# Kernel optimization log

Measured on AMD Instinct MI355X. Metric: run time of the kernel, lower is better.

The kernel has to match this reference:

```python
import jax, jax.numpy as jnp
import numpy as np

B, C, H, W = 64, 1024, 14, 14
DK, DV, NH = 512, 512, 8
NCLS = 32  # each class appears B//NCLS = 2 times -> no singleton labels


def setup_inputs() -> dict:
    key = jax.random.key(0)
    k1, k2, k3, k4 = jax.random.split(key, 4)
    dkh = DK // NH
    x = jax.random.normal(k1, (B, C, H, W), jnp.float32)
    W_qkv = jax.random.normal(k2, (2 * DK + DV, C), jnp.float32) * 0.02
    b_qkv = jnp.zeros((2 * DK + DV,), jnp.float32)
    key_rel_w = jax.random.normal(k3, (2 * W - 1, dkh), jnp.float32)
    key_rel_h = jax.random.normal(k4, (2 * H - 1, dkh), jnp.float32)
    # label-based pair index (training path of the torch module)
    rng = np.random.default_rng(0)
    labels = np.repeat(np.arange(NCLS), B // NCLS)
    rng.shuffle(labels)
    pair = np.empty(B, np.int32)
    for j in range(B):
        idx = np.nonzero(labels == labels[j])[0]
        pos = int(np.nonzero(idx == j)[0][0])
        pair[j] = idx[(pos + 1) % len(idx)]
    return {"x": x, "W_qkv": W_qkv, "b_qkv": b_qkv,
            "key_rel_w": key_rel_w, "key_rel_h": key_rel_h,
            "pair_index": jnp.asarray(pair)}


def rel_to_abs(x):
    b, nh, L, _ = x.shape
    x = jnp.pad(x, ((0, 0), (0, 0), (0, 0), (0, 1)))            # [b,nh,L,2L]
    flat = x.reshape(b, nh, L * 2 * L)
    flat = jnp.pad(flat, ((0, 0), (0, 0), (0, L - 1)))
    return flat.reshape(b, nh, L + 1, 2 * L - 1)[:, :, :L, L - 1:]


def relative_logits_1d(q, rel_k, Hd, Wd, nh, case):
    # q: [b, nh, Hd, Wd, dkh]; rel_k: [2*Wd-1, dkh]
    b = q.shape[0]
    rel = jnp.einsum('bhxyd,md->bhxym', q, rel_k)                 # [b,nh,Hd,Wd,2Wd-1]
    rel = rel_to_abs(rel.reshape(b, nh * Hd, Wd, 2 * Wd - 1))     # [b,nh*Hd,Wd,Wd]
    rel = rel.reshape(b, nh, Hd, Wd, Wd)[:, :, :, None]           # [b,nh,Hd,1,Wd,Wd]
    rel = jnp.broadcast_to(rel, (b, nh, Hd, Hd, Wd, Wd))
    if case == 'w':
        rel = jnp.swapaxes(rel, 3, 4)
    else:  # 'h'
        rel = jnp.swapaxes(rel, 2, 4)
        rel = jnp.swapaxes(rel, 4, 5)
        rel = jnp.swapaxes(rel, 3, 5)
    return rel.reshape(b, nh, Hd * Wd, Hd * Wd)


def reference(x, W_qkv, b_qkv, key_rel_w, key_rel_h, pair_index):
    b, c, h, w = x.shape
    nh, dk, dv = NH, DK, DV
    dkh = dk // nh
    # 1x1 conv == channel GEMM
    qkv = jnp.einsum('bchw,oc->bohw', x, W_qkv) + b_qkv[None, :, None, None]
    q = qkv[:, :dk].reshape(b, nh, dkh, h, w) * dkh ** (-0.5)
    k = qkv[:, dk:2 * dk].reshape(b, nh, dkh, h, w)
    flat_q = q.reshape(b, nh, dkh, h * w)
    flat_k = k.reshape(b, nh, dkh, h * w)
    flat_q = flat_q / jnp.linalg.norm(flat_q, axis=2, keepdims=True)
    flat_k = flat_k / jnp.linalg.norm(flat_k, axis=2, keepdims=True)
    q_avg = (flat_q[pair_index] + flat_q) * 0.5
    logits = jnp.einsum('bndq,bndk->bnqk', q_avg, flat_k)         # [b,nh,HW,HW]
    q_perm = jnp.transpose(q, (0, 1, 3, 4, 2))                    # [b,nh,h,w,dkh]
    w_rel = relative_logits_1d(q_perm, key_rel_w, h, w, nh, 'w')
    h_rel = relative_logits_1d(jnp.swapaxes(q_perm, 2, 3), key_rel_h, w, h, nh, 'h')
    logits = logits + h_rel + w_rel
    # combine_heads + mean over dim 1 == mean over (nh, query) axes
    mean_logits = jnp.mean(logits.reshape(b, nh, h * w, h, w), axis=(1, 2))  # [b,h,w]
    attn = jax.nn.softmax(mean_logits.reshape(b, -1), axis=-1).reshape(b, 1, h, w)
    return jnp.concatenate((x / 49.0, x * attn), axis=1)
```

## Files before the change

### kernel.cpp

```cpp
#include <hip/hip_runtime.h>
#include <hip/hip_bf16.h>
#include <math.h>

typedef unsigned short ushort_t;
using bf16x8 = __attribute__((ext_vector_type(8))) short;
using f32x4  = __attribute__((ext_vector_type(4))) float;

#define BATCH 64
#define CIN   1024
#define HH    14
#define WW    14
#define P     196
#define NHEAD 8
#define DKH   64
#define PPAD  224

#define OFF_Y16  0
#define N_Y16_F  6422528
#define OFF_XB   (OFF_Y16 + N_Y16_F)
#define N_XB_F   7340032
#define OFF_WB   (OFF_XB + N_XB_F)
#define N_WB_F   524288
#define OFF_INK  (OFF_WB + N_WB_F)
#define N_INK    (BATCH*NHEAD*P)
#define OFF_SQ   (OFF_INK + N_INK)
#define N_SQ     (BATCH*NHEAD*DKH)
#define OFF_QHP  (OFF_SQ + N_SQ)
#define N_QHP    (BATCH*NHEAD*HH*DKH)
#define OFF_QWP  (OFF_QHP + N_QHP)
#define N_QWP    (BATCH*NHEAD*WW*DKH)
#define OFF_DOTP (OFF_QWP + N_QWP)
#define N_DOTP   (BATCH*NHEAD*P)
#define OFF_ATTN (OFF_DOTP + N_DOTP)
#define N_ATTN   (BATCH*P)

__device__ __forceinline__ ushort_t f2bf(float f) {
    union { float f; unsigned u; } v; v.f = f;
    unsigned r = v.u + 0x7fffu + ((v.u >> 16) & 1u);
    return (ushort_t)(r >> 16);
}
__device__ __forceinline__ float bf2f(ushort_t u) {
    union { unsigned u; float f; } v; v.u = ((unsigned)u) << 16; return v.f;
}
__device__ __forceinline__ void gll16(const ushort_t* g, ushort_t* l) {
    __builtin_amdgcn_global_load_lds(
        (const __attribute__((address_space(1))) void*)g,
        (__attribute__((address_space(3))) void*)l, 16, 0, 0);
}

__global__ __launch_bounds__(256) void k_convW(const float* __restrict__ Wq,
                                               ushort_t* __restrict__ Wb) {
    int i = blockIdx.x * 256 + threadIdx.x;
    const float4 v = ((const float4*)Wq)[i];
    ushort4 o;
    o.x = f2bf(v.x); o.y = f2bf(v.y); o.z = f2bf(v.z); o.w = f2bf(v.w);
    ((ushort4*)Wb)[i] = o;
}

__global__ __launch_bounds__(256) void k_trans(const float* __restrict__ x,
                                               ushort_t* __restrict__ Xb) {
    const int c0 = blockIdx.x * 64, p0 = blockIdx.y * 32, b = blockIdx.z;
    const int t = threadIdx.x;
    __shared__ float tile[64][33];
    const float* xb = x + (size_t)b * (CIN * P);
#pragma unroll
    for (int it = 0; it < 8; ++it) {
        int idx = t + it * 256;
        int c_l = idx >> 5, p_l = idx & 31;
        int p = p0 + p_l;
        tile[c_l][p_l] = (p < P) ? xb[(size_t)(c0 + c_l) * P + p] : 0.f;
    }
    __syncthreads();
    int c_chunk = (t & 7) * 8, p_l = t >> 3;
    ushort_t buf[8];
#pragma unroll
    for (int e = 0; e < 8; ++e) buf[e] = f2bf(tile[c_chunk + e][p_l]);
    *(uint4*)(Xb + ((size_t)b * PPAD + p0 + p_l) * CIN + c0 + c_chunk) = *(uint4*)buf;
}

__global__ __launch_bounds__(256, 4) void k_mfma(const ushort_t* __restrict__ Xb,
                                                 const ushort_t* __restrict__ Wb,
                                                 const float* __restrict__ bias,
                                                 ushort_t* __restrict__ Y16) {
    const int o0 = blockIdx.x * 128, r0 = blockIdx.y * 128;
    const int tid = threadIdx.x, w = tid >> 6, l = tid & 63;
    const int wm = w >> 1, wn = w & 1;
    __shared__ ushort_t xa[128 * 64];
    __shared__ ushort_t xw[128 * 64];
    f32x4 acc[4][4];
#pragma unroll
    for (int mf = 0; mf < 4; ++mf)
#pragma unroll
        for (int j = 0; j < 4; ++j) acc[mf][j] = (f32x4){0.f, 0.f, 0.f, 0.f};

    const ushort_t* Ab = Xb + (size_t)r0 * CIN;
    const ushort_t* Bb = Wb + (size_t)o0 * CIN;
    const int lrow = l >> 3, lch = (l & 7) * 8;

    for (int c0 = 0; c0 < CIN; c0 += 64) {
        if (c0) __syncthreads();
#pragma unroll
        for (int i = 0; i < 4; ++i) {
            int rowblk = (w * 4 + i) * 8;
            gll16(Ab + (size_t)(rowblk + lrow) * CIN + c0 + lch, xa + rowblk * 64);
        }
#pragma unroll
        for (int i = 0; i < 4; ++i) {
            int rowblk = (w * 4 + i) * 8;
            gll16(Bb + (size_t)(rowblk + lrow) * CIN + c0 + lch, xw + rowblk * 64);
        }
        __syncthreads();
#pragma unroll
        for (int kk = 0; kk < 2; ++kk) {
            bf16x8 bfrag[4];
#pragma unroll
            for (int j = 0; j < 4; ++j)
                bfrag[j] = *(const bf16x8*)(xw + (wn * 64 + j * 16 + (l & 15)) * 64 + kk * 32 + (l >> 4) * 8);
#pragma unroll
            for (int mf = 0; mf < 4; ++mf) {
                bf16x8 afrag = *(const bf16x8*)(xa + (wm * 64 + mf * 16 + (l & 15)) * 64 + kk * 32 + (l >> 4) * 8);
#pragma unroll
                for (int j = 0; j < 4; ++j)
                    acc[mf][j] = __builtin_amdgcn_mfma_f32_16x16x32_bf16(afrag, bfrag[j], acc[mf][j], 0, 0, 0);
            }
        }
    }
    const int oc = l & 15, pq = (l >> 4) * 4;
#pragma unroll
    for (int j = 0; j < 4; ++j) {
        int o = o0 + wn * 64 + j * 16 + oc;
        float bo = bias[o];
#pragma unroll
        for (int mf = 0; mf < 4; ++mf) {
            int r = r0 + wm * 64 + mf * 16 + pq;
            int b = r / PPAD;
            int p = r - b * PPAD;
            if (p < P) {
                ushort_t tmp[4];
#pragma unroll
                for (int e = 0; e < 4; ++e) tmp[e] = f2bf(acc[mf][j][e] + bo);
                *(ushort4*)(Y16 + ((size_t)b * 1024 + o) * P + p) = *(ushort4*)tmp;
            }
        }
    }
}

__global__ __launch_bounds__(256) void k_norm(const ushort_t* __restrict__ Y16,
                                              float* __restrict__ ink_g,
                                              float* __restrict__ sq_g,
                                              float* __restrict__ qhp,
                                              float* __restrict__ qwp) {
    const int bn = blockIdx.x, b = bn >> 3, n = bn & 7;
    const int tid = threadIdx.x;
    __shared__ ushort_t qs[64 * P];
    __shared__ float inq_s[P];
    __shared__ float part[4][64];
    const uint* Yq = (const uint*)(Y16 + ((size_t)b * 1024 + n * 64) * P);
    for (int i = tid; i < 64 * (P / 2); i += 256) ((uint*)qs)[i] = Yq[i];
    const ushort_t* Yk = Y16 + ((size_t)b * 1024 + 512 + n * 64) * P;
    const int p = tid, pc = (p < P) ? p : 0;
    float sk = 0.f;
    for (int d = 0; d < 64; ++d) { float v = bf2f(Yk[d * P + pc]); sk = fmaf(v, v, sk); }
    __syncthreads();
    float sq = 0.f;
    for (int d = 0; d < 64; ++d) { float v = bf2f(qs[d * P + pc]); sq = fmaf(v, v, sq); }
    if (p < P) { ink_g[bn * P + p] = rsqrtf(sk); inq_s[p] = rsqrtf(sq); }
    __syncthreads();
    {
        int d = tid & 63, q4 = tid >> 6;
        float s = 0.f;
        for (int i = 0; i < 49; ++i) {
            int pp = q4 * 49 + i;
            s = fmaf(bf2f(qs[d * P + pp]), inq_s[pp], s);
        }
        part[q4][d] = s;
    }
    __syncthreads();
    if (tid < 64) sq_g[bn * 64 + tid] = part[0][tid] + part[1][tid] + part[2][tid] + part[3][tid];
    for (int it = tid; it < 896; it += 256) {
        int d = it & 63, xx = it >> 6;
        float s = 0.f;
#pragma unroll
        for (int y = 0; y < WW; ++y) s += bf2f(qs[d * P + xx * WW + y]);
        qhp[bn * 896 + it] = s * 0.125f;
    }
    for (int it = tid; it < 896; it += 256) {
        int d = it & 63, y = it >> 6;
        float s = 0.f;
#pragma unroll
        for (int xx = 0; xx < HH; ++xx) s += bf2f(qs[d * P + xx * WW + y]);
        qwp[bn * 896 + it] = s * 0.125f;
    }
}

__global__ __launch_bounds__(256) void k_dot(const ushort_t* __restrict__ Y16,
                                             const float* __restrict__ ink_g,
                                             const float* __restrict__ sq_g,
                                             const int*   __restrict__ pair,
                                             float* __restrict__ dotp) {
    const int bn = blockIdx.x, b = bn >> 3, n = bn & 7;
    const int tid = threadIdx.x;
    __shared__ float Sav[64];
    if (tid < 64) {
        int pb = pair[b];
        Sav[tid] = 0.5f * (sq_g[bn * 64 + tid] + sq_g[(pb * 8 + n) * 64 + tid]);
    }
    __syncthreads();
    const int p = tid;
    if (p < P) {
        const ushort_t* Yk = Y16 + ((size_t)b * 1024 + 512 + n * 64) * P;
        float s = 0.f;
#pragma unroll 8
        for (int d = 0; d < 64; ++d) s = fmaf(Sav[d], bf2f(Yk[d * P + p]), s);
        dotp[bn * P + p] = s * ink_g[bn * P + p];
    }
}

__global__ __launch_bounds__(256) void k_attn2(const float* __restrict__ dotp,
                                               const float* __restrict__ qhp,
                                               const float* __restrict__ qwp,
                                               const float* __restrict__ relw,
                                               const float* __restrict__ relh,
                                               float* __restrict__ attn_g) {
    const int b = blockIdx.x, tid = threadIdx.x;
    __shared__ float qhs[896], qws[896];
    __shared__ float Aw[WW], Ah[HH];
    __shared__ float red[256];
    for (int i = tid; i < 896; i += 256) {
        float sh = 0.f, sw = 0.f;
#pragma unroll
        for (int n = 0; n < 8; ++n) {
            sh += qhp[(size_t)(b * 8 + n) * 896 + i];
            sw += qwp[(size_t)(b * 8 + n) * 896 + i];
        }
        qhs[i] = sh; qws[i] = sw;
    }
    if (tid < WW) { Aw[tid] = 0.f; Ah[tid] = 0.f; }
    __syncthreads();
    if (tid < 196) {
        int X = tid / 14, y = tid % 14;
        const float* qp = &qws[y * 64];
        const float* rw = relw + (13 + X - y) * 64;
        float s = 0.f;
#pragma unroll 8
        for (int d = 0; d < 64; ++d) s = fmaf(qp[d], rw[d], s);
        atomicAdd(&Aw[X], s);
        const float* hp = &qhs[y * 64];
        const float* rh = relh + (13 + X - y) * 64;
        float s2 = 0.f;
#pragma unroll 8
        for (int d = 0; d < 64; ++d) s2 = fmaf(hp[d], rh[d], s2);
        atomicAdd(&Ah[X], s2);
    }
    __syncthreads();
    const int p = tid;
    float v = -1e30f;
    if (p < P) {
        float dot = 0.f;
#pragma unroll
        for (int n = 0; n < 8; ++n) dot += dotp[(size_t)(b * 8 + n) * P + p];
        v = (dot + Ah[p / WW] + Aw[p % WW]) * (1.f / 1568.f);
    }
    red[tid] = v; __syncthreads();
    for (int s = 128; s > 0; s >>= 1) { if (tid < s) red[tid] = fmaxf(red[tid], red[tid + s]); __syncthreads(); }
    float mx = red[0]; __syncthreads();
    float e = (p < P) ? expf(v - mx) : 0.f;
    red[tid] = e; __syncthreads();
    for (int s = 128; s > 0; s >>= 1) { if (tid < s) red[tid] += red[tid + s]; __syncthreads(); }
    if (p < P) attn_g[b * P + p] = e / red[0];
}

__global__ __launch_bounds__(256) void k_out(const float* __restrict__ x,
                                             const float* __restrict__ attn_g,
                                             float* __restrict__ out) {
    const int total4 = BATCH * CIN * P / 4;
    const int stride = gridDim.x * 256;
    const float4* x4 = (const float4*)x;
    const float4* a4 = (const float4*)attn_g;
    float4* o4 = (float4*)out;
    for (int i4 = blockIdx.x * 256 + threadIdx.x; i4 < total4; i4 += stride) {
        int i = i4 * 4;
        int b = i / (CIN * P);
        int r = i - b * (CIN * P);
        int p0 = r % P;
        float4 xv = x4[i4];
        float4 at = a4[(b * P + p0) >> 2];
        float4 o1 = make_float4(xv.x * (1.f/49.f), xv.y * (1.f/49.f),
                                xv.z * (1.f/49.f), xv.w * (1.f/49.f));
        float4 o2 = make_float4(xv.x * at.x, xv.y * at.y, xv.z * at.z, xv.w * at.w);
        o4[(b * (2 * CIN * P) + r) >> 2] = o1;
        o4[(b * (2 * CIN * P) + CIN * P + r) >> 2] = o2;
    }
}

extern "C" void kernel_launch(void* const* d_in, const int* in_sizes, int n_in,
                              void* d_out, int out_size, void* d_ws, size_t ws_size,
                              hipStream_t stream) {
    const float* x    = (const float*)d_in[0];
    const float* Wq   = (const float*)d_in[1];
    const float* bias = (const float*)d_in[2];
    const float* relw = (const float*)d_in[3];
    const float* relh = (const float*)d_in[4];
    const int*   pair = (const int*)d_in[5];
    float* out = (float*)d_out;
    float* ws  = (float*)d_ws;

    ushort_t* Y16 = (ushort_t*)(ws + OFF_Y16);
    ushort_t* Xb  = (ushort_t*)(ws + OFF_XB);
    ushort_t* Wb  = (ushort_t*)(ws + OFF_WB);
    float* ink  = ws + OFF_INK;
    float* sq   = ws + OFF_SQ;
    float* qhp  = ws + OFF_QHP;
    float* qwp  = ws + OFF_QWP;
    float* dotp = ws + OFF_DOTP;
    float* attn = ws + OFF_ATTN;

    k_convW<<<1024, 256, 0, stream>>>(Wq, Wb);
    k_trans<<<dim3(16, 7, 64), 256, 0, stream>>>(x, Xb);
    k_mfma <<<dim3(8, 112), 256, 0, stream>>>(Xb, Wb, bias, Y16);
    k_norm <<<BATCH * NHEAD, 256, 0, stream>>>(Y16, ink, sq, qhp, qwp);
    k_dot  <<<BATCH * NHEAD, 256, 0, stream>>>(Y16, ink, sq, pair, dotp);
    k_attn2<<<BATCH, 256, 0, stream>>>(dotp, qhp, qwp, relw, relh, attn);
    k_out  <<<2048, 256, 0, stream>>>(x, attn, out);
}
```

Measured before the change: 118.6 us.

## Merge weight/input conversion kernels and fuse norm with pair dot product

Combines the weight bf16 conversion and the input transpose into one launch by splitting on block index. It also fuses the normalization and dot kernels: each block now loads its paired sample's query tile and recomputes that tile's normalized sum locally, instead of passing ink/sq through global memory. This removes two launches and a dependency, at the cost of doubling query loads and LDS use per block (about 50KB), which may reduce occupancy.

```diff
diff --git a/kernel.cpp b/kernel.cpp
--- a/kernel.cpp
+++ b/kernel.cpp
@@ -21,11 +21,7 @@
 #define N_XB_F   7340032
 #define OFF_WB   (OFF_XB + N_XB_F)
 #define N_WB_F   524288
-#define OFF_INK  (OFF_WB + N_WB_F)
-#define N_INK    (BATCH*NHEAD*P)
-#define OFF_SQ   (OFF_INK + N_INK)
-#define N_SQ     (BATCH*NHEAD*DKH)
-#define OFF_QHP  (OFF_SQ + N_SQ)
+#define OFF_QHP  (OFF_WB + N_WB_F)
 #define N_QHP    (BATCH*NHEAD*HH*DKH)
 #define OFF_QWP  (OFF_QHP + N_QHP)
 #define N_QWP    (BATCH*NHEAD*WW*DKH)
@@ -48,25 +44,30 @@
         (__attribute__((address_space(3))) void*)l, 16, 0, 0);
 }
 
-__global__ __launch_bounds__(256) void k_convW(const float* __restrict__ Wq,
-                                               ushort_t* __restrict__ Wb) {
-    int i = blockIdx.x * 256 + threadIdx.x;
-    const float4 v = ((const float4*)Wq)[i];
-    ushort4 o;
-    o.x = f2bf(v.x); o.y = f2bf(v.y); o.z = f2bf(v.z); o.w = f2bf(v.w);
-    ((ushort4*)Wb)[i] = o;
-}
-
-__global__ __launch_bounds__(256) void k_trans(const float* __restrict__ x,
-                                               ushort_t* __restrict__ Xb) {
-    const int c0 = blockIdx.x * 64, p0 = blockIdx.y * 32, b = blockIdx.z;
+__global__ __launch_bounds__(256) void k_prep(const float* __restrict__ x,
+                                              const float* __restrict__ Wq,
+                                              ushort_t* __restrict__ Xb,
+                                              ushort_t* __restrict__ Wb) {
+    if (blockIdx.x < 1024) {
+        int i = blockIdx.x * 256 + threadIdx.x;
+        const float4 v = ((const float4*)Wq)[i];
+        ushort4 o;
+        o.x = f2bf(v.x); o.y = f2bf(v.y); o.z = f2bf(v.z); o.w = f2bf(v.w);
+        ((ushort4*)Wb)[i] = o;
+        return;
+    }
+    const int idx = blockIdx.x - 1024;
+    const int c0 = (idx & 15) * 64;
+    const int rest = idx >> 4;
+    const int p0 = (rest % 7) * 32;
+    const int b  = rest / 7;
     const int t = threadIdx.x;
     __shared__ float tile[64][33];
     const float* xb = x + (size_t)b * (CIN * P);
 #pragma unroll
     for (int it = 0; it < 8; ++it) {
-        int idx = t + it * 256;
-        int c_l = idx >> 5, p_l = idx & 31;
+        int id2 = t + it * 256;
+        int c_l = id2 >> 5, p_l = id2 & 31;
         int p = p0 + p_l;
         tile[c_l][p_l] = (p < P) ? xb[(size_t)(c0 + c_l) * P + p] : 0.f;
     }
@@ -145,26 +146,37 @@
     }
 }
 
-__global__ __launch_bounds__(256) void k_norm(const ushort_t* __restrict__ Y16,
-                                              float* __restrict__ ink_g,
-                                              float* __restrict__ sq_g,
-                                              float* __restrict__ qhp,
-                                              float* __restrict__ qwp) {
+__global__ __launch_bounds__(256) void k_normdot(const ushort_t* __restrict__ Y16,
+                                                 const int*   __restrict__ pair,
+                                                 float* __restrict__ qhp,
+                                                 float* __restrict__ qwp,
+                                                 float* __restrict__ dotp) {
     const int bn = blockIdx.x, b = bn >> 3, n = bn & 7;
     const int tid = threadIdx.x;
     __shared__ ushort_t qs[64 * P];
-    __shared__ float inq_s[P];
+    __shared__ ushort_t qp[64 * P];
+    __shared__ float inq_s[P], inqp_s[P];
     __shared__ float part[4][64];
-    const uint* Yq = (const uint*)(Y16 + ((size_t)b * 1024 + n * 64) * P);
-    for (int i = tid; i < 64 * (P / 2); i += 256) ((uint*)qs)[i] = Yq[i];
+    __shared__ float Sav[64];
+    const int pb = pair[b];
+    const uint* Yq  = (const uint*)(Y16 + ((size_t)b  * 1024 + n * 64) * P);
+    const uint* Yqp = (const uint*)(Y16 + ((size_t)pb * 1024 + n * 64) * P);
+    for (int i = tid; i < 64 * (P / 2); i += 256) {
+        ((uint*)qs)[i] = Yq[i];
+        ((uint*)qp)[i] = Yqp[i];
+    }
     const ushort_t* Yk = Y16 + ((size_t)b * 1024 + 512 + n * 64) * P;
     const int p = tid, pc = (p < P) ? p : 0;
     float sk = 0.f;
     for (int d = 0; d < 64; ++d) { float v = bf2f(Yk[d * P + pc]); sk = fmaf(v, v, sk); }
-    __syncthreads();
-    float sq = 0.f;
-    for (int d = 0; d < 64; ++d) { float v = bf2f(qs[d * P + pc]); sq = fmaf(v, v, sq); }
-    if (p < P) { ink_g[bn * P + p] = rsqrtf(sk); inq_s[p] = rsqrtf(sq); }
+    const float inkp = rsqrtf(sk);
+    __syncthreads();
+    float sq = 0.f, sqp = 0.f;
+    for (int d = 0; d < 64; ++d) {
+        float v = bf2f(qs[d * P + pc]); sq  = fmaf(v, v, sq);
+        float u = bf2f(qp[d * P + pc]); sqp = fmaf(u, u, sqp);
+    }
+    if (p < P) { inq_s[p] = rsqrtf(sq); inqp_s[p] = rsqrtf(sqp); }
     __syncthreads();
     {
         int d = tid & 63, q4 = tid >> 6;
@@ -172,11 +184,20 @@
         for (int i = 0; i < 49; ++i) {
             int pp = q4 * 49 + i;
             s = fmaf(bf2f(qs[d * P + pp]), inq_s[pp], s);
+            s = fmaf(bf2f(qp[d * P + pp]), inqp_s[pp], s);
         }
         part[q4][d] = s;
     }
     __syncthreads();
-    if (tid < 64) sq_g[bn * 64 + tid] = part[0][tid] + part[1][tid] + part[2][tid] + part[3][tid];
+    if (tid < 64)
+        Sav[tid] = 0.5f * (part[0][tid] + part[1][tid] + part[2][tid] + part[3][tid]);
+    __syncthreads();
+    if (p < P) {
+        float s = 0.f;
+#pragma unroll 8
+        for (int d = 0; d < 64; ++d) s = fmaf(Sav[d], bf2f(Yk[d * P + p]), s);
+        dotp[bn * P + p] = s * inkp;
+    }
     for (int it = tid; it < 896; it += 256) {
         int d = it & 63, xx = it >> 6;
         float s = 0.f;
@@ -190,29 +211,6 @@
 #pragma unroll
         for (int xx = 0; xx < HH; ++xx) s += bf2f(qs[d * P + xx * WW + y]);
         qwp[bn * 896 + it] = s * 0.125f;
-    }
-}
-
-__global__ __launch_bounds__(256) void k_dot(const ushort_t* __restrict__ Y16,
-                                             const float* __restrict__ ink_g,
-                                             const float* __restrict__ sq_g,
-                                             const int*   __restrict__ pair,
-                                             float* __restrict__ dotp) {
-    const int bn = blockIdx.x, b = bn >> 3, n = bn & 7;
-    const int tid = threadIdx.x;
-    __shared__ float Sav[64];
-    if (tid < 64) {
-        int pb = pair[b];
-        Sav[tid] = 0.5f * (sq_g[bn * 64 + tid] + sq_g[(pb * 8 + n) * 64 + tid]);
-    }
-    __syncthreads();
-    const int p = tid;
-    if (p < P) {
-        const ushort_t* Yk = Y16 + ((size_t)b * 1024 + 512 + n * 64) * P;
-        float s = 0.f;
-#pragma unroll 8
-        for (int d = 0; d < 64; ++d) s = fmaf(Sav[d], bf2f(Yk[d * P + p]), s);
-        dotp[bn * P + p] = s * ink_g[bn * P + p];
     }
 }
 
@@ -308,18 +306,14 @@
     ushort_t* Y16 = (ushort_t*)(ws + OFF_Y16);
     ushort_t* Xb  = (ushort_t*)(ws + OFF_XB);
     ushort_t* Wb  = (ushort_t*)(ws + OFF_WB);
-    float* ink  = ws + OFF_INK;
-    float* sq   = ws + OFF_SQ;
     float* qhp  = ws + OFF_QHP;
     float* qwp  = ws + OFF_QWP;
     float* dotp = ws + OFF_DOTP;
     float* attn = ws + OFF_ATTN;
 
-    k_convW<<<1024, 256, 0, stream>>>(Wq, Wb);
-    k_trans<<<dim3(16, 7, 64), 256, 0, stream>>>(x, Xb);
-    k_mfma <<<dim3(8, 112), 256, 0, stream>>>(Xb, Wb, bias, Y16);
-    k_norm <<<BATCH * NHEAD, 256, 0, stream>>>(Y16, ink, sq, qhp, qwp);
-    k_dot  <<<BATCH * NHEAD, 256, 0, stream>>>(Y16, ink, sq, pair, dotp);
-    k_attn2<<<BATCH, 256, 0, stream>>>(dotp, qhp, qwp, relw, relh, attn);
-    k_out  <<<2048, 256, 0, stream>>>(x, attn, out);
-}
+    k_prep   <<<8192, 256, 0, stream>>>(x, Wq, Xb, Wb);
+    k_mfma   <<<dim3(8, 112), 256, 0, stream>>>(Xb, Wb, bias, Y16);
+    k_normdot<<<BATCH * NHEAD, 256, 0, stream>>>(Y16, pair, qhp, qwp, dotp);
+    k_attn2  <<<BATCH, 256, 0, stream>>>(dotp, qhp, qwp, relw, relh, attn);
+    k_out    <<<2048, 256, 0, stream>>>(x, attn, out);
+}
```

Measured after the change: 114.9 us. 1.03x faster.
